# Performance work log

Hardware: AMD Instinct MI355X
Metric: run time of the kernel (lower is better)

Reference implementation:

```python
import jax, jax.numpy as jnp
import numpy as np
from jax import lax

N = 100000   # num_nodes
E = 1600000  # num_edges (avg degree 16)
F = 128      # num_features
H = 256      # hidden_channels
C = 64       # num_classes
K = 10       # propagation steps
ALPHA = 0.1
BETA = 0.5
THETA = 0.5
EPS = 1e-5   # BatchNorm eps


def setup_inputs() -> dict:
    key = jax.random.key(0)
    ks = jax.random.split(key, 16)
    x = jax.random.normal(ks[0], (N, F), dtype=jnp.float32)
    src = jax.random.randint(ks[1], (E,), 0, N, dtype=jnp.int32)
    dst = jax.random.randint(ks[2], (E,), 0, N, dtype=jnp.int32)
    # row-normalized adjacency weights so repeated A@z stays bounded
    deg = jax.ops.segment_sum(jnp.ones((E,), jnp.float32), dst, num_segments=N)
    w = (1.0 / jnp.maximum(deg, 1.0))[dst]
    # MLP params (Linear + BatchNorm per hidden layer)
    W1 = jax.random.normal(ks[3], (F, H), dtype=jnp.float32) * 0.05
    b1 = jnp.zeros((H,), jnp.float32)
    g1 = jnp.ones((H,), jnp.float32)
    be1 = jnp.zeros((H,), jnp.float32)
    W2 = jax.random.normal(ks[4], (H, H), dtype=jnp.float32) * 0.05
    b2 = jnp.zeros((H,), jnp.float32)
    g2 = jnp.ones((H,), jnp.float32)
    be2 = jnp.zeros((H,), jnp.float32)
    W3 = jax.random.normal(ks[5], (H, C), dtype=jnp.float32) * 0.05
    b3 = jnp.zeros((C,), jnp.float32)
    # lazy caches (warm-start memories); nonzero so the blend branch is taken
    z_sam = jax.random.normal(ks[6], (N, C), dtype=jnp.float32) * 0.1
    g_sam = jax.random.normal(ks[7], (N, C), dtype=jnp.float32) * 0.01
    return dict(x=x, src=src, dst=dst, w=w,
                W1=W1, b1=b1, g1=g1, be1=be1,
                W2=W2, b2=b2, g2=g2, be2=be2,
                W3=W3, b3=b3, z_sam=z_sam, g_sam=g_sam, size=N)


def _bn(h, gamma, beta):
    # BatchNorm1d in training mode: batch statistics over nodes
    mu = jnp.mean(h, axis=0)
    var = jnp.var(h, axis=0)
    return (h - mu) * jax.lax.rsqrt(var + EPS) * gamma + beta


def reference(x, src, dst, w, W1, b1, g1, be1, W2, b2, g2, be2, W3, b3,
              z_sam, g_sam, size):
    # MLP stack: Linear -> BN -> ReLU (dropout omitted: deterministic reference)
    h = jax.nn.relu(_bn(x @ W1 + b1, g1, be1))
    h = jax.nn.relu(_bn(h @ W2 + b2, g2, be2))
    logits = h @ W3 + b3  # [N, C]

    def spmm(z):
        # (A @ z)_i = sum_{j -> i} w_ij * z_j
        return jax.ops.segment_sum(z[src] * w[:, None], dst, num_segments=N)

    # Lazy_Prop.forward: warm-start blend, then K propagation steps
    use_x = jnp.all(z_sam[:size] == 0.0)
    z0 = jnp.where(use_x, logits, (1.0 - BETA) * z_sam + BETA * logits)
    z = lax.fori_loop(0, K, lambda i, z: (1.0 - ALPHA) * spmm(z) + ALPHA * logits, z0)
    return jax.nn.log_softmax(z, axis=1)
```

## Files before the change

kernel.cpp:

```cpp
#include <hip/hip_runtime.h>
#include <hip/hip_bf16.h>

#define NODES 100000
#define EDGES 1600000
#define FEAT  128
#define HID   256
#define CLS   64
#define KPROP 10
#define ALPHA_C 0.1f
#define BETA_C  0.5f
#define BN_EPS  1e-5f

typedef __attribute__((ext_vector_type(8))) short short8;
typedef __attribute__((ext_vector_type(4))) float f32x4;

static __device__ __forceinline__ unsigned short f2b(float f) {
    __hip_bfloat16 h = __float2bfloat16(f);
    return *(unsigned short*)&h;
}
static __device__ __forceinline__ float b2f(unsigned short u) {
    __hip_bfloat16 h;
    *(unsigned short*)&h = u;
    return __bfloat162float(h);
}
static __device__ __forceinline__ float asf(unsigned int u) {
    union { unsigned int u; float f; } c; c.u = u; return c.f;
}

__global__ void packwt_k(const float* __restrict__ W, unsigned short* __restrict__ Wt,
                         int K, int N)
{
    int i = blockIdx.x * 256 + threadIdx.x;
    if (i < K * N) {
        int k = i / N, n = i - k * N;
        Wt[(size_t)n * K + k] = f2b(W[i]);
    }
}

template<bool AF32, bool FUSE, bool STATS, bool OUTF32, int KK, int NCOLG>
__global__ __launch_bounds__(256, 2)
void gemm_lds_k(const void* __restrict__ Ain, const unsigned short* __restrict__ Wt,
                const float* __restrict__ bias,
                const float* __restrict__ scale, const float* __restrict__ shift,
                void* __restrict__ outp,
                float* __restrict__ gsum, float* __restrict__ gsq,
                int M, int N, int nchunks, int nblk)
{
    constexpr int NK8 = KK / 32;
    __shared__ unsigned short Blds[64 * KK];
    __shared__ float Slds[KK];
    __shared__ float Hlds[KK];

    const int lane = threadIdx.x & 63;
    const int wv   = threadIdx.x >> 6;
    const int quad = lane >> 4;
    const int l16  = lane & 15;
    const int colg = (NCOLG > 1) ? (blockIdx.x % NCOLG) : 0;
    const int blk0 = (NCOLG > 1) ? (blockIdx.x / NCOLG) : blockIdx.x;
    const int colbase = colg * 64;

    {
        const unsigned short* wp = Wt + (size_t)colbase * KK;
        constexpr int ELEMS = 64 * KK / 8;
        #pragma unroll
        for (int i0 = 0; i0 < ELEMS; i0 += 256) {
            int i  = i0 + threadIdx.x;
            int c  = i / (KK / 8);
            int k8 = i - c * (KK / 8);
            short8 v = *(const short8*)(wp + (size_t)c * KK + k8 * 8);
            int byte = c * (KK * 2) + ((k8 * 16) ^ ((c & 7) << 4));
            *(short8*)((char*)Blds + byte) = v;
        }
        if constexpr (FUSE) {
            for (int i = threadIdx.x; i < KK; i += 256) {
                Slds[i] = scale[i];
                Hlds[i] = shift[i];
            }
        }
    }
    __syncthreads();

    float bcol[4];
    #pragma unroll
    for (int ct = 0; ct < 4; ++ct) bcol[ct] = bias[colbase + ct * 16 + l16];

    float ps[4] = {0.f, 0.f, 0.f, 0.f};
    float pq[4] = {0.f, 0.f, 0.f, 0.f};

    float4 af0[2][AF32 ? NK8 : 1][2];
    float4 af1[2][AF32 ? NK8 : 1][2];
    short8 ah0[2][AF32 ? 1 : NK8];
    short8 ah1[2][AF32 ? 1 : NK8];

#define LOAD_A(AF, AH, CHK)                                                    \
    if ((CHK) < nchunks) {                                                     \
        const int rb_ = (CHK) * 128 + wv * 32;                                 \
        _Pragma("unroll")                                                      \
        for (int rt = 0; rt < 2; ++rt) {                                       \
            const int row_ = rb_ + rt * 16 + l16;                              \
            const bool ok_ = row_ < M;                                         \
            if constexpr (AF32) {                                              \
                const float* ap_ = (const float*)Ain + (size_t)row_ * KK + quad * 8; \
                _Pragma("unroll")                                              \
                for (int ks = 0; ks < NK8; ++ks) {                             \
                    AF[rt][ks][0] = ok_ ? *(const float4*)(ap_ + ks * 32)                \
                                        : (float4){0.f, 0.f, 0.f, 0.f};        \
                    AF[rt][ks][1] = ok_ ? *(const float4*)(ap_ + ks * 32 + 4)            \
                                        : (float4){0.f, 0.f, 0.f, 0.f};        \
                }                                                              \
            } else {                                                           \
                const unsigned short* ap_ = (const unsigned short*)Ain + (size_t)row_ * KK + quad * 8; \
                _Pragma("unroll")                                              \
                for (int ks = 0; ks < NK8; ++ks)                               \
                    AH[rt][ks] = ok_ ? *(const short8*)(ap_ + ks * 32)         \
                                     : (short8){0, 0, 0, 0, 0, 0, 0, 0};       \
            }                                                                  \
        }                                                                      \
    }

#define COMPUTE(AF, AH, CHK)                                                   \
    {                                                                          \
        const int rb_ = (CHK) * 128 + wv * 32;                                 \
        f32x4 acc[2][4];                                                       \
        _Pragma("unroll")                                                      \
        for (int i = 0; i < 2; ++i)                                            \
            _Pragma("unroll")                                                  \
            for (int j = 0; j < 4; ++j)                                        \
                acc[i][j] = (f32x4){0.f, 0.f, 0.f, 0.f};                       \
        _Pragma("unroll")                                                      \
        for (int ks = 0; ks < NK8; ++ks) {                                     \
            const int k_ = ks * 32 + quad * 8;                                 \
            float sc[8], sh[8];                                                \
            if constexpr (FUSE) {                                              \
                float4 s0 = *(const float4*)&Slds[k_];                         \
                float4 s1 = *(const float4*)&Slds[k_ + 4];                     \
                float4 h0 = *(const float4*)&Hlds[k_];                         \
                float4 h1 = *(const float4*)&Hlds[k_ + 4];                     \
                sc[0]=s0.x; sc[1]=s0.y; sc[2]=s0.z; sc[3]=s0.w;                \
                sc[4]=s1.x; sc[5]=s1.y; sc[6]=s1.z; sc[7]=s1.w;                \
                sh[0]=h0.x; sh[1]=h0.y; sh[2]=h0.z; sh[3]=h0.w;                \
                sh[4]=h1.x; sh[5]=h1.y; sh[6]=h1.z; sh[7]=h1.w;                \
            }                                                                  \
            short8 a2[2];                                                      \
            _Pragma("unroll")                                                  \
            for (int rt = 0; rt < 2; ++rt) {                                   \
                float v[8];                                                    \
                if constexpr (AF32) {                                          \
                    float4 t0 = AF[rt][ks][0];                                 \
                    float4 t1 = AF[rt][ks][1];                                 \
                    v[0]=t0.x; v[1]=t0.y; v[2]=t0.z; v[3]=t0.w;                \
                    v[4]=t1.x; v[5]=t1.y; v[6]=t1.z; v[7]=t1.w;                \
                } else {                                                       \
                    _Pragma("unroll")                                          \
                    for (int j = 0; j < 8; ++j)                                \
                        v[j] = b2f((unsigned short)AH[rt][ks][j]);             \
                }                                                              \
                if constexpr (FUSE) {                                          \
                    _Pragma("unroll")                                          \
                    for (int j = 0; j < 8; ++j)                                \
                        v[j] = fmaxf(fmaf(v[j], sc[j], sh[j]), 0.f);           \
                }                                                              \
                short8 av;                                                     \
                _Pragma("unroll")                                              \
                for (int j = 0; j < 8; ++j) av[j] = (short)f2b(v[j]);          \
                a2[rt] = av;                                                   \
            }                                                                  \
            _Pragma("unroll")                                                  \
            for (int ct = 0; ct < 4; ++ct) {                                   \
                const int boff = (ct * 16 + l16) * (KK * 2)                    \
                               + ((ks * 64 + quad * 16) ^ ((l16 & 7) << 4));   \
                short8 bf = *(const short8*)((const char*)Blds + boff);        \
                acc[0][ct] = __builtin_amdgcn_mfma_f32_16x16x32_bf16(a2[0], bf, acc[0][ct], 0, 0, 0); \
                acc[1][ct] = __builtin_amdgcn_mfma_f32_16x16x32_bf16(a2[1], bf, acc[1][ct], 0, 0, 0); \
            }                                                                  \
        }                                                                      \
        _Pragma("unroll")                                                      \
        for (int ct = 0; ct < 4; ++ct) {                                       \
            const int col_ = colbase + ct * 16 + l16;                          \
            _Pragma("unroll")                                                  \
            for (int rt = 0; rt < 2; ++rt) {                                   \
                _Pragma("unroll")                                              \
                for (int r2 = 0; r2 < 4; ++r2) {                               \
                    const int row_ = rb_ + rt * 16 + quad * 4 + r2;            \
                    if (row_ < M) {                                            \
                        float vv = acc[rt][ct][r2] + bcol[ct];                 \
                        if constexpr (STATS) { ps[ct] += vv; pq[ct] += vv * vv; } \
                        if constexpr (OUTF32) {                                \
                            ((float*)outp)[(size_t)row_ * N + col_] = vv;      \
                        } else {                                               \
                            ((unsigned short*)outp)[(size_t)row_ * N + col_] = f2b(vv); \
                        }                                                      \
                    }                                                          \
                }                                                              \
            }                                                                  \
        }                                                                      \
    }

    int chunk = blk0;
    LOAD_A(af0, ah0, chunk)
    while (chunk < nchunks) {
        const int cn1 = chunk + nblk;
        LOAD_A(af1, ah1, cn1)
        __builtin_amdgcn_sched_barrier(0);
        COMPUTE(af0, ah0, chunk)
        chunk = cn1;
        if (chunk >= nchunks) break;
        const int cn2 = chunk + nblk;
        LOAD_A(af0, ah0, cn2)
        __builtin_amdgcn_sched_barrier(0);
        COMPUTE(af1, ah1, chunk)
        chunk = cn2;
    }
#undef LOAD_A
#undef COMPUTE

    if constexpr (STATS) {
        #pragma unroll
        for (int ct = 0; ct < 4; ++ct) {
            float s = ps[ct];
            s += __shfl_xor(s, 16, 64);
            s += __shfl_xor(s, 32, 64);
            float q = pq[ct];
            q += __shfl_xor(q, 16, 64);
            q += __shfl_xor(q, 32, 64);
            if (lane < 16) {
                atomicAdd(&gsum[colbase + ct * 16 + lane], s);
                atomicAdd(&gsq[colbase + ct * 16 + lane], q);
            }
        }
    }
}

__global__ void bnfin_k(const float* __restrict__ sum, const float* __restrict__ sq,
                        const float* __restrict__ g, const float* __restrict__ be,
                        float* __restrict__ scale, float* __restrict__ shift)
{
    int c = threadIdx.x;
    float mu = sum[c] * (1.f / NODES);
    float var = sq[c] * (1.f / NODES) - mu * mu;
    float sc = g[c] * rsqrtf(var + BN_EPS);
    scale[c] = sc;
    shift[c] = be[c] - mu * sc;
}

__global__ void flag_k(const float* __restrict__ zs, int* __restrict__ flag)
{
    int i = blockIdx.x * 256 + threadIdx.x;
    bool nz = (i < NODES * CLS) && (zs[i] != 0.f);
    if (__any(nz)) {
        if ((threadIdx.x & 63) == 0) *flag = 1;
    }
}

__global__ void blend_k(const float* __restrict__ zs, const float* __restrict__ logits,
                        const int* __restrict__ flag, unsigned short* __restrict__ z0)
{
    int i = blockIdx.x * 256 + threadIdx.x;
    if (i < NODES * CLS) {
        float l = logits[i];
        float v = (*flag) ? ((1.f - BETA_C) * zs[i] + BETA_C * l) : l;
        z0[i] = f2b(v);
    }
}

__global__ void count_k(const int* __restrict__ dst, int* __restrict__ cntx)
{
    int t = blockIdx.x * 256 + threadIdx.x;
    if (t >= EDGES / 4) return;
    int4 d = ((const int4*)dst)[t];
    int* c = cntx + (size_t)(blockIdx.x & 7) * NODES;
    atomicAdd(&c[d.x], 1);
    atomicAdd(&c[d.y], 1);
    atomicAdd(&c[d.z], 1);
    atomicAdd(&c[d.w], 1);
}

__global__ void sumoff_k(int* __restrict__ cntx, int* __restrict__ cnt)
{
    int n = blockIdx.x * 256 + threadIdx.x;
    if (n >= NODES) return;
    int tot = 0;
    int p[8];
    #pragma unroll
    for (int x = 0; x < 8; ++x) {
        p[x] = tot;
        tot += cntx[(size_t)x * NODES + n];
    }
    #pragma unroll
    for (int x = 0; x < 8; ++x)
        cntx[(size_t)x * NODES + n] = p[x];
    cnt[n] = tot;
}

__global__ void scan1_k(const int* __restrict__ cnt, int* __restrict__ rowptr,
                        int* __restrict__ bsum)
{
    __shared__ int s[256];
    int tid = threadIdx.x;
    int i = blockIdx.x * 256 + tid;
    int v = (i < NODES) ? cnt[i] : 0;
    s[tid] = v;
    __syncthreads();
    for (int off = 1; off < 256; off <<= 1) {
        int t = (tid >= off) ? s[tid - off] : 0;
        __syncthreads();
        s[tid] += t;
        __syncthreads();
    }
    if (i < NODES) rowptr[i] = s[tid] - v;
    if (tid == 255) bsum[blockIdx.x] = s[255];
}

__global__ void scan2_k(const int* __restrict__ bsum, int* __restrict__ boffs, int nb)
{
    __shared__ int s[512];
    int tid = threadIdx.x;
    int v = (tid < nb) ? bsum[tid] : 0;
    s[tid] = v;
    __syncthreads();
    for (int off = 1; off < 512; off <<= 1) {
        int t = (tid >= off) ? s[tid - off] : 0;
        __syncthreads();
        s[tid] += t;
        __syncthreads();
    }
    if (tid < nb) boffs[tid] = s[tid] - v;
}

__global__ void scan3_k(int* __restrict__ rowptr, const int* __restrict__ boffs,
                        const int* __restrict__ cntx, int* __restrict__ curx)
{
    int i = blockIdx.x * 256 + threadIdx.x;
    if (i < NODES) {
        int v = rowptr[i] + boffs[blockIdx.x];
        rowptr[i] = v;
        #pragma unroll
        for (int x = 0; x < 8; ++x)
            curx[(size_t)x * NODES + i] = v + cntx[(size_t)x * NODES + i];
    }
    if (i == 0) rowptr[NODES] = EDGES;
}

__global__ void posfill_k(const int* __restrict__ dst, int* __restrict__ curx,
                          int* __restrict__ pos)
{
    int t = blockIdx.x * 256 + threadIdx.x;
    if (t >= EDGES / 4) return;
    int4 d = ((const int4*)dst)[t];
    int* cur = curx + (size_t)(blockIdx.x & 7) * NODES;
    int4 p;
    p.x = atomicAdd(&cur[d.x], 1);
    p.y = atomicAdd(&cur[d.y], 1);
    p.z = atomicAdd(&cur[d.z], 1);
    p.w = atomicAdd(&cur[d.w], 1);
    ((int4*)pos)[t] = p;
}

__global__ void scat_k(const int* __restrict__ src, const int* __restrict__ pos,
                       int* __restrict__ esrc)
{
    int e = blockIdx.x * 256 + threadIdx.x;
    if (e < EDGES) esrc[pos[e]] = src[e];
}

__global__ __launch_bounds__(256)
void prop_k(const int* __restrict__ rowptr, const int* __restrict__ esrc,
            const unsigned long long* __restrict__ zin, const float* __restrict__ logits,
            uint4* __restrict__ zout)
{
    int row = blockIdx.x * 32 + (threadIdx.x >> 3);
    if (row >= NODES) return;
    int l8 = threadIdx.x & 7;
    int beg = rowptr[row], end = rowptr[row + 1];
    float a0 = 0.f, a1 = 0.f, a2 = 0.f, a3 = 0.f;
    float a4 = 0.f, a5 = 0.f, a6 = 0.f, a7 = 0.f;

    for (int cbeg = beg; cbeg < end; cbeg += 16) {
        int e0 = cbeg + l8, e1 = cbeg + 8 + l8;
        int s0 = (e0 < end) ? esrc[e0] : 0;
        int s1 = (e1 < end) ? esrc[e1] : 0;
        int cnt = min(16, end - cbeg);
        if (cnt == 16) {
            int idx[16];
            #pragma unroll
            for (int u = 0; u < 8; ++u) idx[u] = __shfl(s0, u, 8);
            #pragma unroll
            for (int u = 0; u < 8; ++u) idx[8 + u] = __shfl(s1, u, 8);
            unsigned long long vv[32];
            #pragma unroll
            for (int u = 0; u < 16; ++u) {
                const unsigned long long* p = zin + (size_t)idx[u] * 16 + l8 * 2;
                vv[2 * u]     = __hip_atomic_load(p,     __ATOMIC_RELAXED, __HIP_MEMORY_SCOPE_AGENT);
                vv[2 * u + 1] = __hip_atomic_load(p + 1, __ATOMIC_RELAXED, __HIP_MEMORY_SCOPE_AGENT);
            }
            #pragma unroll
            for (int u = 0; u < 16; ++u) {
                unsigned int x0 = (unsigned int)vv[2 * u];
                unsigned int x1 = (unsigned int)(vv[2 * u] >> 32);
                unsigned int x2 = (unsigned int)vv[2 * u + 1];
                unsigned int x3 = (unsigned int)(vv[2 * u + 1] >> 32);
                a0 += asf(x0 << 16);  a1 += asf(x0 & 0xffff0000u);
                a2 += asf(x1 << 16);  a3 += asf(x1 & 0xffff0000u);
                a4 += asf(x2 << 16);  a5 += asf(x2 & 0xffff0000u);
                a6 += asf(x3 << 16);  a7 += asf(x3 & 0xffff0000u);
            }
        } else {
            for (int j = 0; j < cnt; ++j) {
                int sv = (j < 8) ? __shfl(s0, j, 8) : __shfl(s1, j - 8, 8);
                const unsigned long long* p = zin + (size_t)sv * 16 + l8 * 2;
                unsigned long long v0 = __hip_atomic_load(p,     __ATOMIC_RELAXED, __HIP_MEMORY_SCOPE_AGENT);
                unsigned long long v1 = __hip_atomic_load(p + 1, __ATOMIC_RELAXED, __HIP_MEMORY_SCOPE_AGENT);
                unsigned int x0 = (unsigned int)v0;
                unsigned int x1 = (unsigned int)(v0 >> 32);
                unsigned int x2 = (unsigned int)v1;
                unsigned int x3 = (unsigned int)(v1 >> 32);
                a0 += asf(x0 << 16);  a1 += asf(x0 & 0xffff0000u);
                a2 += asf(x1 << 16);  a3 += asf(x1 & 0xffff0000u);
                a4 += asf(x2 << 16);  a5 += asf(x2 & 0xffff0000u);
                a6 += asf(x3 << 16);  a7 += asf(x3 & 0xffff0000u);
            }
        }
    }
    float dg = (float)(end - beg);
    float inv = 1.f / fmaxf(dg, 1.f);
    float cc = (1.f - ALPHA_C) * inv;
    const float* lp = logits + (size_t)row * CLS + l8 * 8;
    float4 lv0 = *(const float4*)lp;
    float4 lv1 = *(const float4*)(lp + 4);
    float r0 = cc * a0 + ALPHA_C * lv0.x;
    float r1 = cc * a1 + ALPHA_C * lv0.y;
    float r2 = cc * a2 + ALPHA_C * lv0.z;
    float r3 = cc * a3 + ALPHA_C * lv0.w;
    float r4 = cc * a4 + ALPHA_C * lv1.x;
    float r5 = cc * a5 + ALPHA_C * lv1.y;
    float r6 = cc * a6 + ALPHA_C * lv1.z;
    float r7 = cc * a7 + ALPHA_C * lv1.w;
    uint4 w;
    w.x = ((unsigned int)f2b(r1) << 16) | (unsigned int)f2b(r0);
    w.y = ((unsigned int)f2b(r3) << 16) | (unsigned int)f2b(r2);
    w.z = ((unsigned int)f2b(r5) << 16) | (unsigned int)f2b(r4);
    w.w = ((unsigned int)f2b(r7) << 16) | (unsigned int)f2b(r6);
    zout[(size_t)row * 8 + l8] = w;
}

__global__ __launch_bounds__(256)
void logsoftmax_k(const unsigned short* __restrict__ z, float* __restrict__ out)
{
    int row = blockIdx.x * 4 + (threadIdx.x >> 6);
    if (row >= NODES) return;
    int lane = threadIdx.x & 63;
    float v = b2f(z[(size_t)row * CLS + lane]);
    float m = v;
    #pragma unroll
    for (int off = 32; off > 0; off >>= 1) m = fmaxf(m, __shfl_xor(m, off, 64));
    float ex = expf(v - m);
    float s = ex;
    #pragma unroll
    for (int off = 32; off > 0; off >>= 1) s += __shfl_xor(s, off, 64);
    out[(size_t)row * CLS + lane] = (v - m) - logf(s);
}

extern "C" void kernel_launch(void* const* d_in, const int* in_sizes, int n_in,
                              void* d_out, int out_size, void* d_ws, size_t ws_size,
                              hipStream_t stream)
{
    const float* x   = (const float*)d_in[0];
    const int*   src = (const int*)d_in[1];
    const int*   dst = (const int*)d_in[2];
    const float* W1  = (const float*)d_in[4];
    const float* b1  = (const float*)d_in[5];
    const float* g1  = (const float*)d_in[6];
    const float* be1 = (const float*)d_in[7];
    const float* W2  = (const float*)d_in[8];
    const float* b2  = (const float*)d_in[9];
    const float* g2  = (const float*)d_in[10];
    const float* be2 = (const float*)d_in[11];
    const float* W3  = (const float*)d_in[12];
    const float* b3  = (const float*)d_in[13];
    const float* zsam = (const float*)d_in[14];
    float* outp = (float*)d_out;

    uint8_t* base = (uint8_t*)d_ws;
    float* s_scale1 = (float*)(base);
    float* s_shift1 = s_scale1 + 256;
    float* s_scale2 = s_shift1 + 256;
    float* s_shift2 = s_scale2 + 256;
    float* s_sum    = s_shift2 + 256;
    float* s_sq     = s_sum + 256;
    int*   flag     = (int*)(s_sq + 256);

    unsigned short* Wt1 = (unsigned short*)(base + (1 << 14));
    unsigned short* Wt2 = Wt1 + (size_t)FEAT * HID;
    unsigned short* Wt3 = Wt2 + (size_t)HID * HID;
    unsigned short* h1  = Wt3 + (size_t)HID * CLS;
    unsigned short* h2  = h1 + (size_t)NODES * HID;
    float* logits = (float*)(h2 + (size_t)NODES * HID);
    unsigned short* zA  = (unsigned short*)(logits + (size_t)NODES * CLS);
    unsigned short* zB  = zA + (size_t)NODES * CLS;
    int* esrc   = (int*)(zB + (size_t)NODES * CLS);
    int* cntx   = esrc + EDGES;
    int* curx   = cntx + (size_t)8 * NODES;
    int* rowptr = curx + (size_t)8 * NODES;
    int* cnt    = rowptr + (NODES + 1);
    int* bsum   = cnt + NODES;
    int* boffs  = bsum + 512;
    int* pos    = (int*)h1;

    const int NCHUNK = (NODES + 127) / 128;
    const int NBLK   = (NCHUNK + 1) / 2;
    const int SCANB  = (NODES + 255) / 256;
    const int EB4    = (EDGES / 4 + 255) / 256;

    packwt_k<<<(FEAT * HID + 255) / 256, 256, 0, stream>>>(W1, Wt1, FEAT, HID);
    packwt_k<<<(HID * HID + 255) / 256, 256, 0, stream>>>(W2, Wt2, HID, HID);
    packwt_k<<<(HID * CLS + 255) / 256, 256, 0, stream>>>(W3, Wt3, HID, CLS);

    hipMemsetAsync(cntx, 0, (size_t)8 * NODES * sizeof(int), stream);
    count_k<<<EB4, 256, 0, stream>>>(dst, cntx);
    sumoff_k<<<SCANB, 256, 0, stream>>>(cntx, cnt);
    scan1_k<<<SCANB, 256, 0, stream>>>(cnt, rowptr, bsum);
    scan2_k<<<1, 512, 0, stream>>>(bsum, boffs, SCANB);
    scan3_k<<<SCANB, 256, 0, stream>>>(rowptr, boffs, cntx, curx);
    posfill_k<<<EB4, 256, 0, stream>>>(dst, curx, pos);
    scat_k<<<EDGES / 256, 256, 0, stream>>>(src, pos, esrc);

    hipMemsetAsync(s_sum, 0, 512 * sizeof(float), stream);
    gemm_lds_k<true, false, true, false, FEAT, 4><<<NBLK * 4, 256, 0, stream>>>(
        x, Wt1, b1, nullptr, nullptr, h1, s_sum, s_sq, NODES, HID, NCHUNK, NBLK);
    bnfin_k<<<1, 256, 0, stream>>>(s_sum, s_sq, g1, be1, s_scale1, s_shift1);

    hipMemsetAsync(s_sum, 0, 512 * sizeof(float), stream);
    gemm_lds_k<false, true, true, false, HID, 4><<<NBLK * 4, 256, 0, stream>>>(
        h1, Wt2, b2, s_scale1, s_shift1, h2, s_sum, s_sq, NODES, HID, NCHUNK, NBLK);
    bnfin_k<<<1, 256, 0, stream>>>(s_sum, s_sq, g2, be2, s_scale2, s_shift2);

    gemm_lds_k<false, true, false, true, HID, 1><<<NBLK, 256, 0, stream>>>(
        h2, Wt3, b3, s_scale2, s_shift2, logits, nullptr, nullptr, NODES, CLS, NCHUNK, NBLK);

    hipMemsetAsync(flag, 0, sizeof(int), stream);
    flag_k<<<(NODES * CLS + 255) / 256, 256, 0, stream>>>(zsam, flag);
    blend_k<<<(NODES * CLS + 255) / 256, 256, 0, stream>>>(zsam, logits, flag, zA);

    const int PROPB = (NODES + 31) / 32;
    for (int it = 0; it < KPROP; ++it) {
        const unsigned long long* zi = (const unsigned long long*)((it & 1) ? zB : zA);
        uint4* zo = (uint4*)((it & 1) ? zA : zB);
        prop_k<<<PROPB, 256, 0, stream>>>(rowptr, esrc, zi, logits, zo);
    }

    logsoftmax_k<<<(NODES + 3) / 4, 256, 0, stream>>>(zA, outp);
}
```

Baseline: 902.4 us.

## Split propagation features into two column halves and add dedicated bf16 first GEMM

The propagation buffers are stored as two planar halves of 32 classes each, and prop_k runs a 2-D grid so each block gathers only 64-byte rows from one half. The intent is a smaller per-pass gather working set that stays in cache better. A separate pass converts x to bf16, and a new gemm1_k keeps the whole W1 tile in LDS (swizzled) and double-buffers A fragments across 32-row chunks. In exchange, esrc and rowptr are read twice per iteration, gathers are narrower, and the x conversion adds an extra pass over the input.

```diff
diff --git a/kernel.cpp b/kernel.cpp
--- a/kernel.cpp
+++ b/kernel.cpp
@@ -34,6 +34,140 @@
     if (i < K * N) {
         int k = i / N, n = i - k * N;
         Wt[(size_t)n * K + k] = f2b(W[i]);
+    }
+}
+
+__global__ void xcvt_k(const float* __restrict__ x, unsigned short* __restrict__ xb)
+{
+    int i = blockIdx.x * 256 + threadIdx.x;
+    if (i < NODES * FEAT / 8) {
+        float4 a = ((const float4*)x)[2 * i];
+        float4 b = ((const float4*)x)[2 * i + 1];
+        short8 o;
+        o[0] = (short)f2b(a.x); o[1] = (short)f2b(a.y);
+        o[2] = (short)f2b(a.z); o[3] = (short)f2b(a.w);
+        o[4] = (short)f2b(b.x); o[5] = (short)f2b(b.y);
+        o[6] = (short)f2b(b.z); o[7] = (short)f2b(b.w);
+        ((short8*)xb)[i] = o;
+    }
+}
+
+__global__ __launch_bounds__(256, 2)
+void gemm1_k(const unsigned short* __restrict__ xb, const unsigned short* __restrict__ Wt,
+             const float* __restrict__ bias, unsigned short* __restrict__ h1,
+             float* __restrict__ gsum, float* __restrict__ gsq,
+             int M, int nchunks, int nblk)
+{
+    __shared__ unsigned short Blds[256 * FEAT];
+    const int lane = threadIdx.x & 63;
+    const int wv   = threadIdx.x >> 6;
+    const int quad = lane >> 4;
+    const int l16  = lane & 15;
+    const int colbase = wv * 64;
+
+    #pragma unroll
+    for (int i0 = 0; i0 < 4096; i0 += 256) {
+        int i  = i0 + threadIdx.x;
+        int c  = i >> 4;
+        int k8 = i & 15;
+        short8 v = *(const short8*)(Wt + (size_t)c * FEAT + k8 * 8);
+        int byte = c * 256 + ((k8 * 16) ^ ((c & 7) << 4));
+        *(short8*)((char*)Blds + byte) = v;
+    }
+    __syncthreads();
+
+    float bcol[4];
+    #pragma unroll
+    for (int ct = 0; ct < 4; ++ct) bcol[ct] = bias[colbase + ct * 16 + l16];
+    float ps[4] = {0.f, 0.f, 0.f, 0.f};
+    float pq[4] = {0.f, 0.f, 0.f, 0.f};
+
+    short8 ah0[2][4], ah1[2][4];
+
+#define LOAD1(AH, CHK)                                                         \
+    if ((CHK) < nchunks) {                                                     \
+        const int rb_ = (CHK) * 32;                                            \
+        _Pragma("unroll")                                                      \
+        for (int rt = 0; rt < 2; ++rt) {                                       \
+            const int row_ = rb_ + rt * 16 + l16;                              \
+            const bool ok_ = row_ < M;                                         \
+            const unsigned short* ap_ = xb + (size_t)row_ * FEAT + quad * 8;   \
+            _Pragma("unroll")                                                  \
+            for (int ks = 0; ks < 4; ++ks)                                     \
+                AH[rt][ks] = ok_ ? *(const short8*)(ap_ + ks * 32)             \
+                                 : (short8){0, 0, 0, 0, 0, 0, 0, 0};           \
+        }                                                                      \
+    }
+
+#define COMP1(AH, CHK)                                                         \
+    {                                                                          \
+        const int rb_ = (CHK) * 32;                                            \
+        f32x4 acc[2][4];                                                       \
+        _Pragma("unroll")                                                      \
+        for (int i = 0; i < 2; ++i)                                            \
+            _Pragma("unroll")                                                  \
+            for (int j = 0; j < 4; ++j)                                        \
+                acc[i][j] = (f32x4){0.f, 0.f, 0.f, 0.f};                       \
+        _Pragma("unroll")                                                      \
+        for (int ks = 0; ks < 4; ++ks) {                                       \
+            _Pragma("unroll")                                                  \
+            for (int ct = 0; ct < 4; ++ct) {                                   \
+                const int col_ = colbase + ct * 16 + l16;                      \
+                const int boff = col_ * 256                                    \
+                               + ((ks * 64 + quad * 16) ^ ((col_ & 7) << 4));  \
+                short8 bf = *(const short8*)((const char*)Blds + boff);        \
+                acc[0][ct] = __builtin_amdgcn_mfma_f32_16x16x32_bf16(AH[0][ks], bf, acc[0][ct], 0, 0, 0); \
+                acc[1][ct] = __builtin_amdgcn_mfma_f32_16x16x32_bf16(AH[1][ks], bf, acc[1][ct], 0, 0, 0); \
+            }                                                                  \
+        }                                                                      \
+        _Pragma("unroll")                                                      \
+        for (int ct = 0; ct < 4; ++ct) {                                       \
+            const int col_ = colbase + ct * 16 + l16;                          \
+            _Pragma("unroll")                                                  \
+            for (int rt = 0; rt < 2; ++rt) {                                   \
+                _Pragma("unroll")                                              \
+                for (int r2 = 0; r2 < 4; ++r2) {                               \
+                    const int row_ = rb_ + rt * 16 + quad * 4 + r2;            \
+                    if (row_ < M) {                                            \
+                        float vv = acc[rt][ct][r2] + bcol[ct];                 \
+                        ps[ct] += vv; pq[ct] += vv * vv;                       \
+                        h1[(size_t)row_ * HID + col_] = f2b(vv);               \
+                    }                                                          \
+                }                                                              \
+            }                                                                  \
+        }                                                                      \
+    }
+
+    int chunk = blockIdx.x;
+    LOAD1(ah0, chunk)
+    while (chunk < nchunks) {
+        const int cn1 = chunk + nblk;
+        LOAD1(ah1, cn1)
+        __builtin_amdgcn_sched_barrier(0);
+        COMP1(ah0, chunk)
+        chunk = cn1;
+        if (chunk >= nchunks) break;
+        const int cn2 = chunk + nblk;
+        LOAD1(ah0, cn2)
+        __builtin_amdgcn_sched_barrier(0);
+        COMP1(ah1, chunk)
+        chunk = cn2;
+    }
+#undef LOAD1
+#undef COMP1
+
+    #pragma unroll
+    for (int ct = 0; ct < 4; ++ct) {
+        float s = ps[ct];
+        s += __shfl_xor(s, 16, 64);
+        s += __shfl_xor(s, 32, 64);
+        float q = pq[ct];
+        q += __shfl_xor(q, 16, 64);
+        q += __shfl_xor(q, 32, 64);
+        if (lane < 16) {
+            atomicAdd(&gsum[colbase + ct * 16 + lane], s);
+            atomicAdd(&gsq[colbase + ct * 16 + lane], q);
+        }
     }
 }
 
@@ -259,7 +393,8 @@
     if (i < NODES * CLS) {
         float l = logits[i];
         float v = (*flag) ? ((1.f - BETA_C) * zs[i] + BETA_C * l) : l;
-        z0[i] = f2b(v);
+        int row = i >> 6, c = i & 63, p = c >> 5;
+        z0[((size_t)p * NODES + row) * 32 + (c & 31)] = f2b(v);
     }
 }
 
@@ -368,37 +503,42 @@
             const unsigned long long* __restrict__ zin, const float* __restrict__ logits,
             uint4* __restrict__ zout)
 {
-    int row = blockIdx.x * 32 + (threadIdx.x >> 3);
+    const int p = blockIdx.y;
+    int row = blockIdx.x * 64 + (threadIdx.x >> 2);
     if (row >= NODES) return;
-    int l8 = threadIdx.x & 7;
+    int l4 = threadIdx.x & 3;
     int beg = rowptr[row], end = rowptr[row + 1];
+    const unsigned long long* zp = zin + (size_t)p * NODES * 8;
     float a0 = 0.f, a1 = 0.f, a2 = 0.f, a3 = 0.f;
     float a4 = 0.f, a5 = 0.f, a6 = 0.f, a7 = 0.f;
 
     for (int cbeg = beg; cbeg < end; cbeg += 16) {
-        int e0 = cbeg + l8, e1 = cbeg + 8 + l8;
-        int s0 = (e0 < end) ? esrc[e0] : 0;
-        int s1 = (e1 < end) ? esrc[e1] : 0;
         int cnt = min(16, end - cbeg);
+        int eb = cbeg + l4 * 4;
+        int s0 = (eb     < end) ? esrc[eb]     : 0;
+        int s1 = (eb + 1 < end) ? esrc[eb + 1] : 0;
+        int s2 = (eb + 2 < end) ? esrc[eb + 2] : 0;
+        int s3 = (eb + 3 < end) ? esrc[eb + 3] : 0;
         if (cnt == 16) {
             int idx[16];
             #pragma unroll
-            for (int u = 0; u < 8; ++u) idx[u] = __shfl(s0, u, 8);
-            #pragma unroll
-            for (int u = 0; u < 8; ++u) idx[8 + u] = __shfl(s1, u, 8);
+            for (int j = 0; j < 16; ++j) {
+                int sv = (j & 3) == 0 ? s0 : (j & 3) == 1 ? s1 : (j & 3) == 2 ? s2 : s3;
+                idx[j] = __shfl(sv, j >> 2, 4);
+            }
             unsigned long long vv[32];
             #pragma unroll
-            for (int u = 0; u < 16; ++u) {
-                const unsigned long long* p = zin + (size_t)idx[u] * 16 + l8 * 2;
-                vv[2 * u]     = __hip_atomic_load(p,     __ATOMIC_RELAXED, __HIP_MEMORY_SCOPE_AGENT);
-                vv[2 * u + 1] = __hip_atomic_load(p + 1, __ATOMIC_RELAXED, __HIP_MEMORY_SCOPE_AGENT);
+            for (int j = 0; j < 16; ++j) {
+                const unsigned long long* bp = zp + (size_t)idx[j] * 8 + l4 * 2;
+                vv[2 * j]     = __hip_atomic_load(bp,     __ATOMIC_RELAXED, __HIP_MEMORY_SCOPE_AGENT);
+                vv[2 * j + 1] = __hip_atomic_load(bp + 1, __ATOMIC_RELAXED, __HIP_MEMORY_SCOPE_AGENT);
             }
             #pragma unroll
-            for (int u = 0; u < 16; ++u) {
-                unsigned int x0 = (unsigned int)vv[2 * u];
-                unsigned int x1 = (unsigned int)(vv[2 * u] >> 32);
-                unsigned int x2 = (unsigned int)vv[2 * u + 1];
-                unsigned int x3 = (unsigned int)(vv[2 * u + 1] >> 32);
+            for (int j = 0; j < 16; ++j) {
+                unsigned int x0 = (unsigned int)vv[2 * j];
+                unsigned int x1 = (unsigned int)(vv[2 * j] >> 32);
+                unsigned int x2 = (unsigned int)vv[2 * j + 1];
+                unsigned int x3 = (unsigned int)(vv[2 * j + 1] >> 32);
                 a0 += asf(x0 << 16);  a1 += asf(x0 & 0xffff0000u);
                 a2 += asf(x1 << 16);  a3 += asf(x1 & 0xffff0000u);
                 a4 += asf(x2 << 16);  a5 += asf(x2 & 0xffff0000u);
@@ -406,10 +546,11 @@
             }
         } else {
             for (int j = 0; j < cnt; ++j) {
-                int sv = (j < 8) ? __shfl(s0, j, 8) : __shfl(s1, j - 8, 8);
-                const unsigned long long* p = zin + (size_t)sv * 16 + l8 * 2;
-                unsigned long long v0 = __hip_atomic_load(p,     __ATOMIC_RELAXED, __HIP_MEMORY_SCOPE_AGENT);
-                unsigned long long v1 = __hip_atomic_load(p + 1, __ATOMIC_RELAXED, __HIP_MEMORY_SCOPE_AGENT);
+                int sv = (j & 3) == 0 ? s0 : (j & 3) == 1 ? s1 : (j & 3) == 2 ? s2 : s3;
+                int id = __shfl(sv, j >> 2, 4);
+                const unsigned long long* bp = zp + (size_t)id * 8 + l4 * 2;
+                unsigned long long v0 = __hip_atomic_load(bp,     __ATOMIC_RELAXED, __HIP_MEMORY_SCOPE_AGENT);
+                unsigned long long v1 = __hip_atomic_load(bp + 1, __ATOMIC_RELAXED, __HIP_MEMORY_SCOPE_AGENT);
                 unsigned int x0 = (unsigned int)v0;
                 unsigned int x1 = (unsigned int)(v0 >> 32);
                 unsigned int x2 = (unsigned int)v1;
@@ -424,7 +565,7 @@
     float dg = (float)(end - beg);
     float inv = 1.f / fmaxf(dg, 1.f);
     float cc = (1.f - ALPHA_C) * inv;
-    const float* lp = logits + (size_t)row * CLS + l8 * 8;
+    const float* lp = logits + (size_t)row * CLS + p * 32 + l4 * 8;
     float4 lv0 = *(const float4*)lp;
     float4 lv1 = *(const float4*)(lp + 4);
     float r0 = cc * a0 + ALPHA_C * lv0.x;
@@ -440,7 +581,7 @@
     w.y = ((unsigned int)f2b(r3) << 16) | (unsigned int)f2b(r2);
     w.z = ((unsigned int)f2b(r5) << 16) | (unsigned int)f2b(r4);
     w.w = ((unsigned int)f2b(r7) << 16) | (unsigned int)f2b(r6);
-    zout[(size_t)row * 8 + l8] = w;
+    zout[((size_t)p * NODES + row) * 4 + l4] = w;
 }
 
 __global__ __launch_bounds__(256)
@@ -449,7 +590,8 @@
     int row = blockIdx.x * 4 + (threadIdx.x >> 6);
     if (row >= NODES) return;
     int lane = threadIdx.x & 63;
-    float v = b2f(z[(size_t)row * CLS + lane]);
+    int p = lane >> 5;
+    float v = b2f(z[((size_t)p * NODES + row) * 32 + (lane & 31)]);
     float m = v;
     #pragma unroll
     for (int off = 32; off > 0; off >>= 1) m = fmaxf(m, __shfl_xor(m, off, 64));
@@ -504,16 +646,20 @@
     int* cnt    = rowptr + (NODES + 1);
     int* bsum   = cnt + NODES;
     int* boffs  = bsum + 512;
-    int* pos    = (int*)h1;
+    int* pos = (int*)h1;
+    unsigned short* xb = h2;
 
     const int NCHUNK = (NODES + 127) / 128;
     const int NBLK   = (NCHUNK + 1) / 2;
+    const int NCH1   = (NODES + 31) / 32;
+    const int NB1    = 512;
     const int SCANB  = (NODES + 255) / 256;
     const int EB4    = (EDGES / 4 + 255) / 256;
 
     packwt_k<<<(FEAT * HID + 255) / 256, 256, 0, stream>>>(W1, Wt1, FEAT, HID);
     packwt_k<<<(HID * HID + 255) / 256, 256, 0, stream>>>(W2, Wt2, HID, HID);
     packwt_k<<<(HID * CLS + 255) / 256, 256, 0, stream>>>(W3, Wt3, HID, CLS);
+    xcvt_k<<<(NODES * FEAT / 8 + 255) / 256, 256, 0, stream>>>(x, xb);
 
     hipMemsetAsync(cntx, 0, (size_t)8 * NODES * sizeof(int), stream);
     count_k<<<EB4, 256, 0, stream>>>(dst, cntx);
@@ -525,8 +671,7 @@
     scat_k<<<EDGES / 256, 256, 0, stream>>>(src, pos, esrc);
 
     hipMemsetAsync(s_sum, 0, 512 * sizeof(float), stream);
-    gemm_lds_k<true, false, true, false, FEAT, 4><<<NBLK * 4, 256, 0, stream>>>(
-        x, Wt1, b1, nullptr, nullptr, h1, s_sum, s_sq, NODES, HID, NCHUNK, NBLK);
+    gemm1_k<<<NB1, 256, 0, stream>>>(xb, Wt1, b1, h1, s_sum, s_sq, NODES, NCH1, NB1);
     bnfin_k<<<1, 256, 0, stream>>>(s_sum, s_sq, g1, be1, s_scale1, s_shift1);
 
     hipMemsetAsync(s_sum, 0, 512 * sizeof(float), stream);
@@ -541,11 +686,11 @@
     flag_k<<<(NODES * CLS + 255) / 256, 256, 0, stream>>>(zsam, flag);
     blend_k<<<(NODES * CLS + 255) / 256, 256, 0, stream>>>(zsam, logits, flag, zA);
 
-    const int PROPB = (NODES + 31) / 32;
+    const dim3 PGRID((NODES + 63) / 64, 2);
     for (int it = 0; it < KPROP; ++it) {
         const unsigned long long* zi = (const unsigned long long*)((it & 1) ? zB : zA);
         uint4* zo = (uint4*)((it & 1) ? zA : zB);
-        prop_k<<<PROPB, 256, 0, stream>>>(rowptr, esrc, zi, logits, zo);
+        prop_k<<<PGRID, 256, 0, stream>>>(rowptr, esrc, zi, logits, zo);
     }
 
     logsoftmax_k<<<(NODES + 3) / 4, 256, 0, stream>>>(zA, outp);
```

Result: slower. 1.013 ms (+12.3%).
